# Kernel tuning notes

Hardware: AMD Instinct MI355X
Metric: run time of the kernel (lower is better)

Reference implementation:

```python
import jax, jax.numpy as jnp
import numpy as np
from jax import lax

B, C_IN, C_OUT, H, W, K, MID = 16, 256, 256, 64, 64, 3, 64
BN_EPS = 1e-5


def setup_inputs() -> dict:
    key = jax.random.key(0)
    ks = jax.random.split(key, 16)
    inp = {
        'x': jax.random.normal(ks[0], (B, C_IN, H, W), dtype=jnp.float32),
        # 4 kernel banks: (4, c2, c1//g, k, k)
        'weight': jax.random.normal(ks[1], (4, C_OUT, C_IN, K, K), dtype=jnp.float32) * 0.05,
        'gamma': jnp.ones((C_OUT,), jnp.float32),
        'beta': jnp.zeros((C_OUT,), jnp.float32),
    }
    # four attention branches: Linear(c, mid, bias=False) -> ReLU -> Linear(mid, 4, bias=True)
    names = ['s', 'c', 'f', 'w']
    for i, n in enumerate(names):
        inp[f'fc_{n}_w1'] = jax.random.normal(ks[2 + 3 * i], (MID, C_IN), dtype=jnp.float32) * 0.05
        inp[f'fc_{n}_w2'] = jax.random.normal(ks[3 + 3 * i], (4, MID), dtype=jnp.float32) * 0.05
        inp[f'fc_{n}_b2'] = jax.random.normal(ks[4 + 3 * i], (4,), dtype=jnp.float32) * 0.05
    return inp


def _branch(pooled, w1, w2, b2):
    # pooled: [B, C]; w1: [MID, C]; w2: [4, MID]
    h = jax.nn.relu(pooled @ w1.T)
    return jax.nn.softmax(h @ w2.T + b2, axis=1)  # [B, 4]


def reference(x, weight, gamma, beta,
              fc_s_w1, fc_s_w2, fc_s_b2,
              fc_c_w1, fc_c_w2, fc_c_b2,
              fc_f_w1, fc_f_w2, fc_f_b2,
              fc_w_w1, fc_w_w2, fc_w_b2):
    b = x.shape[0]
    pooled = jnp.mean(x, axis=(2, 3))  # GAP -> [B, C]
    alpha = (_branch(pooled, fc_s_w1, fc_s_w2, fc_s_b2)
             * _branch(pooled, fc_c_w1, fc_c_w2, fc_c_b2)
             * _branch(pooled, fc_f_w1, fc_f_w2, fc_f_b2)
             * _branch(pooled, fc_w_w1, fc_w_w2, fc_w_b2))  # [B, 4]
    # per-sample dynamic kernels: [B, out_c, in_c, k, k]
    dyn_w = jnp.einsum('bn,noikl->boikl', alpha, weight)

    def conv_one(xi, wi):
        # xi: [C, H, W]; wi: [out_c, in_c, k, k]
        return lax.conv_general_dilated(
            xi[None], wi, window_strides=(1, 1), padding='SAME',
            dimension_numbers=('NCHW', 'OIHW', 'NCHW'))[0]

    out = jax.vmap(conv_one)(x, dyn_w)  # [B, out_c, H, W]

    # BatchNorm2d (training-mode batch statistics)
    mean = jnp.mean(out, axis=(0, 2, 3))
    var = jnp.var(out, axis=(0, 2, 3))
    out = (out - mean[None, :, None, None]) * jax.lax.rsqrt(var + BN_EPS)[None, :, None, None]
    return out * gamma[None, :, None, None] + beta[None, :, None, None]
```

## Files before the change

### kernel.cpp

```cpp
#include <hip/hip_runtime.h>
#include <math.h>

#define BB 16
#define CIN 256
#define COUT 256
#define HH 64
#define WW 64
#define NBANK_STRIDE 589824

typedef short bf16x8 __attribute__((ext_vector_type(8)));
typedef float f32x4 __attribute__((ext_vector_type(4)));

#define WS_XT_OFF 32768
#define WS_DW_OFF 33587200
#define WS_NEED   52461568ULL

static __device__ __forceinline__ short f2bf(float f) {
    union { float f; unsigned u; } v; v.f = f;
    unsigned r = v.u + 0x7FFF + ((v.u >> 16) & 1);
    return (short)(r >> 16);
}

struct AttnParams {
    const float* w1[4];
    const float* w2[4];
    const float* b2[4];
};

__global__ __launch_bounds__(256) void xpose_kernel(const float* __restrict__ x,
                                                    short* __restrict__ xT,
                                                    float* __restrict__ pooled) {
    const int ci0 = blockIdx.x * 32;
    const int h0 = blockIdx.y * 4;
    const int b = blockIdx.z;
    const int t = threadIdx.x;
    __shared__ __align__(16) short tile[64][40];
    const int ci = t >> 3;
    const int l = t & 7;
    const int w = t >> 2;
    const int s4 = t & 3;
    float sacc = 0.f;
    for (int hh = 0; hh < 4; ++hh) {
        const int h = h0 + hh;
        __syncthreads();
        {
            const float4* src = (const float4*)(x + ((size_t)(b * 256 + ci0 + ci)) * 4096 + h * 64);
            float4 v1 = src[l * 2];
            float4 v2 = src[l * 2 + 1];
            tile[l * 8 + 0][ci] = f2bf(v1.x);
            tile[l * 8 + 1][ci] = f2bf(v1.y);
            tile[l * 8 + 2][ci] = f2bf(v1.z);
            tile[l * 8 + 3][ci] = f2bf(v1.w);
            tile[l * 8 + 4][ci] = f2bf(v2.x);
            tile[l * 8 + 5][ci] = f2bf(v2.y);
            tile[l * 8 + 6][ci] = f2bf(v2.z);
            tile[l * 8 + 7][ci] = f2bf(v2.w);
            sacc += v1.x + v1.y + v1.z + v1.w + v2.x + v2.y + v2.z + v2.w;
        }
        __syncthreads();
        {
            bf16x8 val = *(const bf16x8*)&tile[w][s4 * 8];
            *(bf16x8*)&xT[((size_t)b * 4096 + h * 64 + w) * 256 + ci0 + s4 * 8] = val;
        }
    }
    sacc += __shfl_xor(sacc, 1, 64);
    sacc += __shfl_xor(sacc, 2, 64);
    sacc += __shfl_xor(sacc, 4, 64);
    if (l == 0) atomicAdd(&pooled[b * 256 + ci0 + ci], sacc);
}

__global__ __launch_bounds__(256) void attn_kernel(AttnParams p, float* __restrict__ ws_f) {
    const int b = blockIdx.x;
    const int t = threadIdx.x;
    const int wv = t >> 6;
    const int lane = t & 63;
    __shared__ float ps[256];
    __shared__ float hs[4][64];
    __shared__ float lg[4][4];
    __shared__ float sm[4][4];
    ws_f[4096 + b * 256 + t] = 0.f;
    ps[t] = ws_f[b * 256 + t] * (1.0f / 4096.0f);
    __syncthreads();
    {
        const float4* w1v = (const float4*)(p.w1[wv] + lane * 256);
        float h = 0.f;
#pragma unroll 8
        for (int i = 0; i < 64; ++i) {
            float4 w4 = w1v[i];
            h += w4.x * ps[i * 4 + 0] + w4.y * ps[i * 4 + 1] +
                 w4.z * ps[i * 4 + 2] + w4.w * ps[i * 4 + 3];
        }
        hs[wv][lane] = fmaxf(h, 0.f);
    }
    __syncthreads();
    if (t < 16) {
        const int n = t >> 2, j = t & 3;
        const float* w2 = p.w2[n];
        float l = p.b2[n][j];
        for (int m = 0; m < 64; ++m) l += w2[j * 64 + m] * hs[n][m];
        lg[n][j] = l;
    }
    __syncthreads();
    if (t < 4) {
        const int n = t;
        float mx = fmaxf(fmaxf(lg[n][0], lg[n][1]), fmaxf(lg[n][2], lg[n][3]));
        float e0 = expf(lg[n][0] - mx), e1 = expf(lg[n][1] - mx);
        float e2 = expf(lg[n][2] - mx), e3 = expf(lg[n][3] - mx);
        float inv = 1.f / (e0 + e1 + e2 + e3);
        sm[n][0] = e0 * inv; sm[n][1] = e1 * inv; sm[n][2] = e2 * inv; sm[n][3] = e3 * inv;
    }
    __syncthreads();
    if (t < 4) ws_f[b * 256 + t] = sm[0][t] * sm[1][t] * sm[2][t] * sm[3][t];
}

__global__ __launch_bounds__(256) void dynw_kernel(const float* __restrict__ wt,
                                                   const float* __restrict__ ws_f,
                                                   short* __restrict__ dynwF) {
    const int co = blockIdx.x;
    const int ci = threadIdx.x;
    const int cotile = co >> 4;
    const int mh = co & 15;
    __shared__ __align__(16) short st[9][272];
    float w[4][9];
#pragma unroll
    for (int n = 0; n < 4; ++n) {
        const size_t base = ((size_t)(n * 256 + co) * 256 + ci) * 9;
#pragma unroll
        for (int k = 0; k < 9; ++k) w[n][k] = wt[base + k];
    }
    for (int b = 0; b < BB; ++b) {
        const float a0 = ws_f[b * 256 + 0];
        const float a1 = ws_f[b * 256 + 1];
        const float a2 = ws_f[b * 256 + 2];
        const float a3 = ws_f[b * 256 + 3];
#pragma unroll
        for (int k = 0; k < 9; ++k)
            st[k][ci] = f2bf(a0 * w[0][k] + a1 * w[1][k] + a2 * w[2][k] + a3 * w[3][k]);
        __syncthreads();
#pragma unroll
        for (int i = 0; i < 2; ++i) {
            const int task = ci + 256 * i;
            if (task < 288) {
                const int k = task >> 5;
                const int c5 = task & 31;
                const int cc = c5 >> 2;
                const int q = c5 & 3;
                bf16x8 v = *(const bf16x8*)&st[k][cc * 32 + q * 8];
                *(bf16x8*)&dynwF[((size_t)((b * 9 + k) * 16 + cotile) << 12) + cc * 512 + q * 128 + mh * 8] = v;
            }
        }
        __syncthreads();
    }
}

__global__ __launch_bounds__(256, 2) void conv_mfma_kernel(const short* __restrict__ xT,
                                                           const short* __restrict__ dynwF,
                                                           float* __restrict__ out,
                                                           float* __restrict__ bn_part) {
    const int id = blockIdx.x;
    const int xcd = id & 7;
    const int wi = id >> 3;
    const int b = xcd + ((wi >> 5) << 3);
    const int rem = wi & 31;
    const int mt = rem >> 4;
    const int nt = rem & 15;

    const int t = threadIdx.x;
    const int lane = t & 63;
    const int wv = t >> 6;
    const int wx = wv & 1;
    const int wy = wv >> 1;
    const int mh = lane & 15;
    const int q = lane >> 4;
    const int r0 = nt * 4;
    const int co0 = mt * 128;

    __shared__ __align__(16) short xs[396 * 64];
    __shared__ __align__(16) short As[2][4096];
    __shared__ float red[128][2][2];

    f32x4 acc[4][8];
#pragma unroll
    for (int i = 0; i < 4; ++i)
#pragma unroll
        for (int j = 0; j < 8; ++j) acc[i][j] = (f32x4){0.f, 0.f, 0.f, 0.f};

    const size_t a_b9 = (size_t)b * 9;
    const int a_ct = mt * 8 + (t >> 5);
    const int a_port16 = (t & 31) * 16;
    const int a_dst = (t >> 5) * 512 + a_port16;
    const int a_rd0 = (wy * 4) * 512 + lane * 8;

    const bf16x8 zero8 = {0, 0, 0, 0, 0, 0, 0, 0};

    for (int cc = 0; cc < 8; ++cc) {
        const int ci0 = cc * 32;
        __syncthreads();
        const short* asrc0 = dynwF + ((((a_b9 + 0) * 16 + a_ct) * 8 + cc) << 9) + a_port16;
        bf16x8 pa0 = *(const bf16x8*)(asrc0);
        bf16x8 pa1 = *(const bf16x8*)(asrc0 + 8);
#pragma unroll
        for (int i = 0; i < 7; ++i) {
            int idx = t + 256 * i;
            if (idx < 1584) {
                int p = idx >> 2;
                int sub = idx & 3;
                int lr = p / 66;
                int lc = p - lr * 66;
                int r = r0 - 1 + lr;
                int c = lc - 1;
                bf16x8 v = zero8;
                if ((unsigned)r < 64u && (unsigned)c < 64u)
                    v = *(const bf16x8*)&xT[((size_t)b * 4096 + r * 64 + c) * 256 + ci0 + sub * 8];
                *(bf16x8*)&xs[(p << 6) + ((sub ^ (p & 7)) << 3)] = v;
            }
        }
        *(bf16x8*)&As[0][a_dst] = pa0;
        *(bf16x8*)&As[0][a_dst + 8] = pa1;
        __syncthreads();
#pragma unroll
        for (int khw = 0; khw < 9; ++khw) {
            const int kh = khw / 3;
            const int kw = khw - kh * 3;
            bf16x8 na0, na1;
            if (khw < 8) {
                const short* s = dynwF + ((((a_b9 + khw + 1) * 16 + a_ct) * 8 + cc) << 9) + a_port16;
                na0 = *(const bf16x8*)(s);
                na1 = *(const bf16x8*)(s + 8);
            }
            bf16x8 bfr[8];
#pragma unroll
            for (int ni = 0; ni < 8; ++ni) {
                const int row_l = wx * 2 + (ni >> 2) + kh;
                const int col_l = (ni & 3) * 16 + kw + mh;
                const int pp = row_l * 66 + col_l;
                bfr[ni] = *(const bf16x8*)&xs[(pp << 6) + ((q ^ (pp & 7)) << 3)];
            }
#pragma unroll
            for (int mi = 0; mi < 4; ++mi) {
                bf16x8 af = *(const bf16x8*)&As[khw & 1][a_rd0 + mi * 512];
#pragma unroll
                for (int ni = 0; ni < 8; ++ni)
                    acc[mi][ni] = __builtin_amdgcn_mfma_f32_16x16x32_bf16(af, bfr[ni], acc[mi][ni], 0, 0, 0);
            }
            if (khw < 8) {
                *(bf16x8*)&As[(khw + 1) & 1][a_dst] = na0;
                *(bf16x8*)&As[(khw + 1) & 1][a_dst + 8] = na1;
                __syncthreads();
            }
        }
    }

    float s16[4][4], q16[4][4];
#pragma unroll
    for (int mi = 0; mi < 4; ++mi)
#pragma unroll
        for (int reg = 0; reg < 4; ++reg) { s16[mi][reg] = 0.f; q16[mi][reg] = 0.f; }

#pragma unroll
    for (int mi = 0; mi < 4; ++mi) {
#pragma unroll
        for (int ni = 0; ni < 8; ++ni) {
            const int pix = wx * 128 + ni * 16 + mh;
            const int h = r0 + (pix >> 6);
            const int w = pix & 63;
#pragma unroll
            for (int reg = 0; reg < 4; ++reg) {
                const int co = co0 + wy * 64 + mi * 16 + q * 4 + reg;
                const float e = acc[mi][ni][reg];
                out[(((size_t)b * 256 + co) << 12) + (h << 6) + w] = e;
                s16[mi][reg] += e;
                q16[mi][reg] += e * e;
            }
        }
    }
#pragma unroll
    for (int mi = 0; mi < 4; ++mi)
#pragma unroll
        for (int reg = 0; reg < 4; ++reg) {
            float s = s16[mi][reg], sq = q16[mi][reg];
            s += __shfl_xor(s, 1, 64);  sq += __shfl_xor(sq, 1, 64);
            s += __shfl_xor(s, 2, 64);  sq += __shfl_xor(sq, 2, 64);
            s += __shfl_xor(s, 4, 64);  sq += __shfl_xor(sq, 4, 64);
            s += __shfl_xor(s, 8, 64);  sq += __shfl_xor(sq, 8, 64);
            if (mh == 0) {
                const int co_l = wy * 64 + mi * 16 + q * 4 + reg;
                red[co_l][0][wx] = s;
                red[co_l][1][wx] = sq;
            }
        }
    __syncthreads();
    {
        const int co_l = t >> 1;
        const int st = t & 1;
        float v = red[co_l][st][0] + red[co_l][st][1];
        atomicAdd(&bn_part[(st * 256 + co0 + co_l) * 8 + (nt & 7)], v);
    }
}

__global__ __launch_bounds__(256) void bn_apply_kernel(float* __restrict__ out,
                                                       const float* __restrict__ bn_part,
                                                       const float* __restrict__ gamma,
                                                       const float* __restrict__ beta) {
    const int gid = blockIdx.x * 256 + threadIdx.x;
    const int c = (blockIdx.x >> 2) & 255;
    float S = 0.f, Q = 0.f;
#pragma unroll
    for (int s = 0; s < 8; ++s) {
        S += bn_part[c * 8 + s];
        Q += bn_part[(256 + c) * 8 + s];
    }
    const float mean = S * (1.f / 65536.f);
    const float var = Q * (1.f / 65536.f) - mean * mean;
    const float inv = rsqrtf(var + 1e-5f);
    const float sc = gamma[c] * inv;
    const float sh = beta[c] - mean * sc;
    float4* p = (float4*)out;
    float4 v = p[gid];
    v.x = v.x * sc + sh;
    v.y = v.y * sc + sh;
    v.z = v.z * sc + sh;
    v.w = v.w * sc + sh;
    p[gid] = v;
}

__global__ __launch_bounds__(256) void gap_kernel(const float* __restrict__ x,
                                                  float* __restrict__ pooled) {
    const int plane = blockIdx.x;
    const float4* p = (const float4*)(x + (size_t)plane * 4096);
    const int t = threadIdx.x;
    float s = 0.f;
#pragma unroll
    for (int i = 0; i < 4; ++i) {
        float4 v = p[t + 256 * i];
        s += v.x + v.y + v.z + v.w;
    }
#pragma unroll
    for (int off = 32; off > 0; off >>= 1) s += __shfl_down(s, off, 64);
    __shared__ float red[4];
    if ((t & 63) == 0) red[t >> 6] = s;
    __syncthreads();
    if (t == 0) pooled[plane] = (red[0] + red[1] + red[2] + red[3]) * (1.0f / 4096.0f);
}

__global__ __launch_bounds__(64) void attn64_kernel(const float* __restrict__ pooled,
                                                    AttnParams p,
                                                    float* __restrict__ alpha) {
    const int b = blockIdx.x;
    const int t = threadIdx.x;
    __shared__ float ps[256];
    __shared__ float hs[64];
    __shared__ float lg[4];
    __shared__ float prod[4];
#pragma unroll
    for (int i = 0; i < 4; ++i) ps[t + 64 * i] = pooled[b * 256 + t + 64 * i];
    if (t < 4) prod[t] = 1.f;
    __syncthreads();
    for (int n = 0; n < 4; ++n) {
        const float* w1 = p.w1[n];
        float h = 0.f;
        for (int c = 0; c < 256; ++c) h += w1[t * 256 + c] * ps[c];
        hs[t] = fmaxf(h, 0.f);
        __syncthreads();
        if (t < 4) {
            const float* w2 = p.w2[n];
            float l = p.b2[n][t];
            for (int m = 0; m < 64; ++m) l += w2[t * 64 + m] * hs[m];
            lg[t] = l;
        }
        __syncthreads();
        if (t == 0) {
            float mx = fmaxf(fmaxf(lg[0], lg[1]), fmaxf(lg[2], lg[3]));
            float e0 = expf(lg[0] - mx), e1 = expf(lg[1] - mx);
            float e2 = expf(lg[2] - mx), e3 = expf(lg[3] - mx);
            float inv = 1.f / (e0 + e1 + e2 + e3);
            prod[0] *= e0 * inv; prod[1] *= e1 * inv;
            prod[2] *= e2 * inv; prod[3] *= e3 * inv;
        }
        __syncthreads();
    }
    if (t < 4) alpha[b * 4 + t] = prod[t];
}

__global__ __launch_bounds__(256) void conv_fp32_kernel(const float* __restrict__ x,
                                                        const float* __restrict__ wt,
                                                        const float* __restrict__ alpha,
                                                        float* __restrict__ out) {
    const int h = blockIdx.x;
    const int cot = blockIdx.y;
    const int b = blockIdx.z;
    const int t = threadIdx.x;
    const int tx = t & 15;
    const int ty = t >> 4;
    const int co0 = cot * 64;
    __shared__ __align__(16) float xsf[32][68];
    __shared__ __align__(16) float wshf[3][32][68];
    const float a0 = alpha[b * 4 + 0], a1 = alpha[b * 4 + 1];
    const float a2 = alpha[b * 4 + 2], a3 = alpha[b * 4 + 3];
    float acc[4][4];
#pragma unroll
    for (int i = 0; i < 4; ++i)
#pragma unroll
        for (int j = 0; j < 4; ++j) acc[i][j] = 0.f;
    const size_t xbase = (size_t)b * CIN * 4096;
    for (int kh = 0; kh < 3; ++kh) {
        const int r = h + kh - 1;
        if (r < 0 || r >= HH) continue;
        for (int chunk = 0; chunk < 8; ++chunk) {
            const int ci0 = chunk * 32;
            __syncthreads();
#pragma unroll
            for (int i = 0; i < 8; ++i) {
                int flat = t + 256 * i;
                int ci = flat >> 6;
                int w = flat & 63;
                xsf[ci][1 + w] = x[xbase + (size_t)(ci0 + ci) * 4096 + r * 64 + w];
            }
            if (t < 32) { xsf[t][0] = 0.f; xsf[t][65] = 0.f; xsf[t][66] = 0.f; xsf[t][67] = 0.f; }
#pragma unroll
            for (int j = 0; j < 24; ++j) {
                int e = t + 256 * j;
                int co = e / 96;
                int rem = e - co * 96;
                int ci = rem / 3;
                int kw = rem - ci * 3;
                size_t g = (((size_t)(co0 + co) * 256 + (ci0 + ci)) * 3 + kh) * 3 + kw;
                wshf[kw][ci][co] = a0 * wt[g] + a1 * wt[g + NBANK_STRIDE] +
                                   a2 * wt[g + 2 * NBANK_STRIDE] + a3 * wt[g + 3 * NBANK_STRIDE];
            }
            __syncthreads();
            for (int ci = 0; ci < 32; ++ci) {
                float4 w0 = *(const float4*)&wshf[0][ci][tx * 4];
                float4 w1v = *(const float4*)&wshf[1][ci][tx * 4];
                float4 w2v = *(const float4*)&wshf[2][ci][tx * 4];
                float4 xa = *(const float4*)&xsf[ci][ty * 4];
                float4 xb = *(const float4*)&xsf[ci][ty * 4 + 4];
                float v[8] = {xa.x, xa.y, xa.z, xa.w, xb.x, xb.y, xb.z, xb.w};
                float aw[3][4] = {{w0.x, w0.y, w0.z, w0.w},
                                  {w1v.x, w1v.y, w1v.z, w1v.w},
                                  {w2v.x, w2v.y, w2v.z, w2v.w}};
#pragma unroll
                for (int kw = 0; kw < 3; ++kw)
#pragma unroll
                    for (int i = 0; i < 4; ++i)
#pragma unroll
                        for (int j = 0; j < 4; ++j)
                            acc[i][j] += aw[kw][i] * v[j + kw];
            }
        }
    }
    size_t obase = (((size_t)b * COUT + co0 + tx * 4) * 64 + h) * 64 + ty * 4;
#pragma unroll
    for (int i = 0; i < 4; ++i) {
        float4 o = {acc[i][0], acc[i][1], acc[i][2], acc[i][3]};
        *(float4*)&out[obase + (size_t)i * 4096] = o;
    }
}

__global__ __launch_bounds__(256) void bn_stats_kernel(const float* __restrict__ out,
                                                       const float* __restrict__ gamma,
                                                       const float* __restrict__ beta,
                                                       float* __restrict__ scale,
                                                       float* __restrict__ shift) {
    const int co = blockIdx.x;
    const int t = threadIdx.x;
    float s = 0.f, sq = 0.f;
    for (int b = 0; b < BB; ++b) {
        const float4* p = (const float4*)(out + ((size_t)b * 256 + co) * 4096);
#pragma unroll
        for (int i = 0; i < 4; ++i) {
            float4 v = p[t + 256 * i];
            s += v.x + v.y + v.z + v.w;
            sq += v.x * v.x + v.y * v.y + v.z * v.z + v.w * v.w;
        }
    }
#pragma unroll
    for (int off = 32; off > 0; off >>= 1) {
        s += __shfl_down(s, off, 64);
        sq += __shfl_down(sq, off, 64);
    }
    __shared__ float rs[4], rq[4];
    if ((t & 63) == 0) { rs[t >> 6] = s; rq[t >> 6] = sq; }
    __syncthreads();
    if (t == 0) {
        float S = rs[0] + rs[1] + rs[2] + rs[3];
        float Q = rq[0] + rq[1] + rq[2] + rq[3];
        float mean = S * (1.f / 65536.f);
        float var = Q * (1.f / 65536.f) - mean * mean;
        float inv = rsqrtf(var + 1e-5f);
        float sc = gamma[co] * inv;
        scale[co] = sc;
        shift[co] = beta[co] - mean * sc;
    }
}

__global__ __launch_bounds__(256) void bn_apply_sc_kernel(float* __restrict__ out,
                                                          const float* __restrict__ scale,
                                                          const float* __restrict__ shift) {
    const int gid = blockIdx.x * 256 + threadIdx.x;
    const int c = (gid >> 10) & 255;
    float4* p = (float4*)out;
    float4 v = p[gid];
    const float sc = scale[c], sh = shift[c];
    v.x = v.x * sc + sh;
    v.y = v.y * sc + sh;
    v.z = v.z * sc + sh;
    v.w = v.w * sc + sh;
    p[gid] = v;
}

extern "C" void kernel_launch(void* const* d_in, const int* in_sizes, int n_in,
                              void* d_out, int out_size, void* d_ws, size_t ws_size,
                              hipStream_t stream) {
    (void)in_sizes; (void)n_in; (void)out_size;
    const float* x = (const float*)d_in[0];
    const float* wt = (const float*)d_in[1];
    const float* gamma = (const float*)d_in[2];
    const float* beta = (const float*)d_in[3];
    AttnParams ap;
    for (int n = 0; n < 4; ++n) {
        ap.w1[n] = (const float*)d_in[4 + 3 * n];
        ap.w2[n] = (const float*)d_in[5 + 3 * n];
        ap.b2[n] = (const float*)d_in[6 + 3 * n];
    }
    float* ws_f = (float*)d_ws;
    float* out = (float*)d_out;

    if (ws_size >= WS_NEED) {
        short* xT = (short*)((char*)d_ws + WS_XT_OFF);
        short* dynwF = (short*)((char*)d_ws + WS_DW_OFF);
        float* bn_part = ws_f + 4096;

        hipMemsetAsync(d_ws, 0, 32768, stream);
        xpose_kernel<<<dim3(8, 16, 16), 256, 0, stream>>>(x, xT, ws_f);
        attn_kernel<<<16, 256, 0, stream>>>(ap, ws_f);
        dynw_kernel<<<256, 256, 0, stream>>>(wt, ws_f, dynwF);
        conv_mfma_kernel<<<512, 256, 0, stream>>>(xT, dynwF, out, bn_part);
        bn_apply_kernel<<<16384, 256, 0, stream>>>(out, bn_part, gamma, beta);
    } else {
        float* pooled = ws_f;
        float* alpha = ws_f + 4096;
        float* scale = ws_f + 4160;
        float* shift = ws_f + 4416;
        gap_kernel<<<4096, 256, 0, stream>>>(x, pooled);
        attn64_kernel<<<16, 64, 0, stream>>>(pooled, ap, alpha);
        conv_fp32_kernel<<<dim3(64, 4, 16), 256, 0, stream>>>(x, wt, alpha, out);
        bn_stats_kernel<<<256, 256, 0, stream>>>(out, gamma, beta, scale, shift);
        bn_apply_sc_kernel<<<16384, 256, 0, stream>>>(out, scale, shift);
    }
}
```

Measured before the change: 272.3 us.

## Fuse BatchNorm apply into conv kernel via grid-wide atomic barrier

The conv kernel now holds its accumulators in registers, publishes per-channel sum and sum-of-squares partials, then waits on a global atomic counter until all 512 blocks have contributed. Each block then computes the scale and shift for its channels and writes the normalized output directly. This removes the separate bn_apply pass, which read and wrote the whole 64 MB output a second time. The grid barrier assumes all 512 blocks are co-resident (2 per CU on 256 CUs), which risks deadlock if occupancy is lower. The counter lives in a workspace slot that is zeroed by the memset and also cleared in attn_kernel.

Result: slower. 291.0 us (+6.9%).

```diff
diff --git a/kernel.cpp b/kernel.cpp
--- a/kernel.cpp
+++ b/kernel.cpp
@@ -81,6 +81,7 @@
     ws_f[4096 + b * 256 + t] = 0.f;
     ps[t] = ws_f[b * 256 + t] * (1.0f / 4096.0f);
     __syncthreads();
+    if (b == 0 && t == 8) ws_f[8] = 0.f;
     {
         const float4* w1v = (const float4*)(p.w1[wv] + lane * 256);
         float h = 0.f;
@@ -156,7 +157,10 @@
 __global__ __launch_bounds__(256, 2) void conv_mfma_kernel(const short* __restrict__ xT,
                                                            const short* __restrict__ dynwF,
                                                            float* __restrict__ out,
-                                                           float* __restrict__ bn_part) {
+                                                           float* __restrict__ bn_part,
+                                                           const float* __restrict__ gamma,
+                                                           const float* __restrict__ beta,
+                                                           int* __restrict__ cnt) {
     const int id = blockIdx.x;
     const int xcd = id & 7;
     const int wi = id >> 3;
@@ -258,22 +262,15 @@
         for (int reg = 0; reg < 4; ++reg) { s16[mi][reg] = 0.f; q16[mi][reg] = 0.f; }
 
 #pragma unroll
-    for (int mi = 0; mi < 4; ++mi) {
-#pragma unroll
-        for (int ni = 0; ni < 8; ++ni) {
-            const int pix = wx * 128 + ni * 16 + mh;
-            const int h = r0 + (pix >> 6);
-            const int w = pix & 63;
+    for (int mi = 0; mi < 4; ++mi)
+#pragma unroll
+        for (int ni = 0; ni < 8; ++ni)
 #pragma unroll
             for (int reg = 0; reg < 4; ++reg) {
-                const int co = co0 + wy * 64 + mi * 16 + q * 4 + reg;
                 const float e = acc[mi][ni][reg];
-                out[(((size_t)b * 256 + co) << 12) + (h << 6) + w] = e;
                 s16[mi][reg] += e;
                 q16[mi][reg] += e * e;
             }
-        }
-    }
 #pragma unroll
     for (int mi = 0; mi < 4; ++mi)
 #pragma unroll
@@ -296,32 +293,49 @@
         float v = red[co_l][st][0] + red[co_l][st][1];
         atomicAdd(&bn_part[(st * 256 + co0 + co_l) * 8 + (nt & 7)], v);
     }
-}
-
-__global__ __launch_bounds__(256) void bn_apply_kernel(float* __restrict__ out,
-                                                       const float* __restrict__ bn_part,
-                                                       const float* __restrict__ gamma,
-                                                       const float* __restrict__ beta) {
-    const int gid = blockIdx.x * 256 + threadIdx.x;
-    const int c = (blockIdx.x >> 2) & 255;
-    float S = 0.f, Q = 0.f;
-#pragma unroll
-    for (int s = 0; s < 8; ++s) {
-        S += bn_part[c * 8 + s];
-        Q += bn_part[(256 + c) * 8 + s];
-    }
-    const float mean = S * (1.f / 65536.f);
-    const float var = Q * (1.f / 65536.f) - mean * mean;
-    const float inv = rsqrtf(var + 1e-5f);
-    const float sc = gamma[c] * inv;
-    const float sh = beta[c] - mean * sc;
-    float4* p = (float4*)out;
-    float4 v = p[gid];
-    v.x = v.x * sc + sh;
-    v.y = v.y * sc + sh;
-    v.z = v.z * sc + sh;
-    v.w = v.w * sc + sh;
-    p[gid] = v;
+    __syncthreads();
+
+    if (t == 0) {
+        __threadfence();
+        atomicAdd(cnt, 1);
+        while (__hip_atomic_load(cnt, __ATOMIC_ACQUIRE, __HIP_MEMORY_SCOPE_AGENT) < 512)
+            __builtin_amdgcn_s_sleep(8);
+    }
+    __syncthreads();
+
+    float* scsh = &red[0][0][0];
+    if (t < 128) {
+        const int co = co0 + t;
+        float S = 0.f, Q = 0.f;
+#pragma unroll
+        for (int s = 0; s < 8; ++s) {
+            S += __hip_atomic_load(&bn_part[co * 8 + s], __ATOMIC_RELAXED, __HIP_MEMORY_SCOPE_AGENT);
+            Q += __hip_atomic_load(&bn_part[(256 + co) * 8 + s], __ATOMIC_RELAXED, __HIP_MEMORY_SCOPE_AGENT);
+        }
+        const float mean = S * (1.f / 65536.f);
+        const float var = Q * (1.f / 65536.f) - mean * mean;
+        const float inv = rsqrtf(var + 1e-5f);
+        const float sc = gamma[co] * inv;
+        scsh[t * 2] = sc;
+        scsh[t * 2 + 1] = beta[co] - mean * sc;
+    }
+    __syncthreads();
+
+#pragma unroll
+    for (int mi = 0; mi < 4; ++mi) {
+#pragma unroll
+        for (int ni = 0; ni < 8; ++ni) {
+            const int pix = wx * 128 + ni * 16 + mh;
+            const int h = r0 + (pix >> 6);
+            const int w = pix & 63;
+#pragma unroll
+            for (int reg = 0; reg < 4; ++reg) {
+                const int co_l = wy * 64 + mi * 16 + q * 4 + reg;
+                const float e = acc[mi][ni][reg] * scsh[co_l * 2] + scsh[co_l * 2 + 1];
+                out[(((size_t)b * 256 + co0 + co_l) << 12) + (h << 6) + w] = e;
+            }
+        }
+    }
 }
 
 __global__ __launch_bounds__(256) void gap_kernel(const float* __restrict__ x,
@@ -530,13 +544,13 @@
         short* xT = (short*)((char*)d_ws + WS_XT_OFF);
         short* dynwF = (short*)((char*)d_ws + WS_DW_OFF);
         float* bn_part = ws_f + 4096;
+        int* cnt = (int*)(ws_f + 8);
 
         hipMemsetAsync(d_ws, 0, 32768, stream);
         xpose_kernel<<<dim3(8, 16, 16), 256, 0, stream>>>(x, xT, ws_f);
         attn_kernel<<<16, 256, 0, stream>>>(ap, ws_f);
         dynw_kernel<<<256, 256, 0, stream>>>(wt, ws_f, dynwF);
-        conv_mfma_kernel<<<512, 256, 0, stream>>>(xT, dynwF, out, bn_part);
-        bn_apply_kernel<<<16384, 256, 0, stream>>>(out, bn_part, gamma, beta);
+        conv_mfma_kernel<<<512, 256, 0, stream>>>(xT, dynwF, out, bn_part, gamma, beta, cnt);
     } else {
         float* pooled = ws_f;
         float* alpha = ws_f + 4096;
```

## Load dynamic-weight fragments directly to registers, drop LDS A staging

Applied to the files above, without the earlier changes.

The weight (A) operand was previously staged through a double-buffered LDS tile with a barrier after every kernel tap. It is now loaded straight from global memory into registers, using two register sets in ping-pong with a two-tap prefetch distance. This removes eight barriers per channel chunk and the LDS write/read traffic for A. In exchange it uses more VGPRs and relies on the weight layout being arranged so each lane's fragment is contiguous, with the global load latency now hidden only by the MFMA work of the preceding taps.

New measurement: 393.7 us. 1.45x slower.

```diff
diff --git a/kernel.cpp b/kernel.cpp
--- a/kernel.cpp
+++ b/kernel.cpp
@@ -176,7 +176,6 @@
     const int co0 = mt * 128;
 
     __shared__ __align__(16) short xs[396 * 64];
-    __shared__ __align__(16) short As[2][4096];
     __shared__ float red[128][2][2];
 
     f32x4 acc[4][8];
@@ -186,70 +185,87 @@
         for (int j = 0; j < 8; ++j) acc[i][j] = (f32x4){0.f, 0.f, 0.f, 0.f};
 
     const size_t a_b9 = (size_t)b * 9;
-    const int a_ct = mt * 8 + (t >> 5);
-    const int a_port16 = (t & 31) * 16;
-    const int a_dst = (t >> 5) * 512 + a_port16;
-    const int a_rd0 = (wy * 4) * 512 + lane * 8;
+    const int a_cot0 = mt * 8 + wy * 4;
+    const short* Aw = dynwF + lane * 8;
+
+#define LOAD_A(dst, k, c)                                                             \
+    {                                                                                 \
+        _Pragma("unroll")                                                             \
+        for (int mi = 0; mi < 4; ++mi)                                                \
+            dst[mi] = *(const bf16x8*)(Aw + ((((a_b9 + (k)) * 16 + a_cot0 + mi) * 8 + (c)) << 9)); \
+    }
+
+    bf16x8 afA[4], afB[4];
+    LOAD_A(afA, 0, 0);
+    LOAD_A(afB, 1, 0);
 
     const bf16x8 zero8 = {0, 0, 0, 0, 0, 0, 0, 0};
 
-    for (int cc = 0; cc < 8; ++cc) {
-        const int ci0 = cc * 32;
-        __syncthreads();
-        const short* asrc0 = dynwF + ((((a_b9 + 0) * 16 + a_ct) * 8 + cc) << 9) + a_port16;
-        bf16x8 pa0 = *(const bf16x8*)(asrc0);
-        bf16x8 pa1 = *(const bf16x8*)(asrc0 + 8);
-#pragma unroll
-        for (int i = 0; i < 7; ++i) {
-            int idx = t + 256 * i;
-            if (idx < 1584) {
-                int p = idx >> 2;
-                int sub = idx & 3;
-                int lr = p / 66;
-                int lc = p - lr * 66;
-                int r = r0 - 1 + lr;
-                int c = lc - 1;
-                bf16x8 v = zero8;
-                if ((unsigned)r < 64u && (unsigned)c < 64u)
-                    v = *(const bf16x8*)&xT[((size_t)b * 4096 + r * 64 + c) * 256 + ci0 + sub * 8];
-                *(bf16x8*)&xs[(p << 6) + ((sub ^ (p & 7)) << 3)] = v;
-            }
-        }
-        *(bf16x8*)&As[0][a_dst] = pa0;
-        *(bf16x8*)&As[0][a_dst + 8] = pa1;
-        __syncthreads();
-#pragma unroll
-        for (int khw = 0; khw < 9; ++khw) {
-            const int kh = khw / 3;
-            const int kw = khw - kh * 3;
-            bf16x8 na0, na1;
-            if (khw < 8) {
-                const short* s = dynwF + ((((a_b9 + khw + 1) * 16 + a_ct) * 8 + cc) << 9) + a_port16;
-                na0 = *(const bf16x8*)(s);
-                na1 = *(const bf16x8*)(s + 8);
-            }
-            bf16x8 bfr[8];
-#pragma unroll
-            for (int ni = 0; ni < 8; ++ni) {
-                const int row_l = wx * 2 + (ni >> 2) + kh;
-                const int col_l = (ni & 3) * 16 + kw + mh;
-                const int pp = row_l * 66 + col_l;
-                bfr[ni] = *(const bf16x8*)&xs[(pp << 6) + ((q ^ (pp & 7)) << 3)];
-            }
-#pragma unroll
-            for (int mi = 0; mi < 4; ++mi) {
-                bf16x8 af = *(const bf16x8*)&As[khw & 1][a_rd0 + mi * 512];
-#pragma unroll
-                for (int ni = 0; ni < 8; ++ni)
-                    acc[mi][ni] = __builtin_amdgcn_mfma_f32_16x16x32_bf16(af, bfr[ni], acc[mi][ni], 0, 0, 0);
-            }
-            if (khw < 8) {
-                *(bf16x8*)&As[(khw + 1) & 1][a_dst] = na0;
-                *(bf16x8*)&As[(khw + 1) & 1][a_dst + 8] = na1;
-                __syncthreads();
-            }
-        }
-    }
+    for (int ccp = 0; ccp < 4; ++ccp) {
+#pragma unroll
+        for (int half = 0; half < 2; ++half) {
+            const int cc = ccp * 2 + half;
+            const int ci0 = cc * 32;
+            __syncthreads();
+#pragma unroll
+            for (int i = 0; i < 7; ++i) {
+                int idx = t + 256 * i;
+                if (idx < 1584) {
+                    int p = idx >> 2;
+                    int sub = idx & 3;
+                    int lr = p / 66;
+                    int lc = p - lr * 66;
+                    int r = r0 - 1 + lr;
+                    int c = lc - 1;
+                    bf16x8 v = zero8;
+                    if ((unsigned)r < 64u && (unsigned)c < 64u)
+                        v = *(const bf16x8*)&xT[((size_t)b * 4096 + r * 64 + c) * 256 + ci0 + sub * 8];
+                    *(bf16x8*)&xs[(p << 6) + ((sub ^ (p & 7)) << 3)] = v;
+                }
+            }
+            __syncthreads();
+#pragma unroll
+            for (int khw = 0; khw < 9; ++khw) {
+                const int kh = khw / 3;
+                const int kw = khw - kh * 3;
+                const int par = (half + khw) & 1;
+
+                bf16x8 bfr[8];
+#pragma unroll
+                for (int ni = 0; ni < 8; ++ni) {
+                    const int row_l = wx * 2 + (ni >> 2) + kh;
+                    const int col_l = (ni & 3) * 16 + kw + mh;
+                    const int pp = row_l * 66 + col_l;
+                    bfr[ni] = *(const bf16x8*)&xs[(pp << 6) + ((q ^ (pp & 7)) << 3)];
+                }
+
+                if (par == 0) {
+#pragma unroll
+                    for (int mi = 0; mi < 4; ++mi)
+#pragma unroll
+                        for (int ni = 0; ni < 8; ++ni)
+                            acc[mi][ni] = __builtin_amdgcn_mfma_f32_16x16x32_bf16(afA[mi], bfr[ni], acc[mi][ni], 0, 0, 0);
+                    if (!(cc == 7 && khw >= 7)) {
+                        const int nk = (khw < 7) ? (khw + 2) : (khw - 7);
+                        const int ncc = (khw < 7) ? cc : (cc + 1);
+                        LOAD_A(afA, nk, ncc);
+                    }
+                } else {
+#pragma unroll
+                    for (int mi = 0; mi < 4; ++mi)
+#pragma unroll
+                        for (int ni = 0; ni < 8; ++ni)
+                            acc[mi][ni] = __builtin_amdgcn_mfma_f32_16x16x32_bf16(afB[mi], bfr[ni], acc[mi][ni], 0, 0, 0);
+                    if (!(cc == 7 && khw >= 7)) {
+                        const int nk = (khw < 7) ? (khw + 2) : (khw - 7);
+                        const int ncc = (khw < 7) ? cc : (cc + 1);
+                        LOAD_A(afB, nk, ncc);
+                    }
+                }
+            }
+        }
+    }
+#undef LOAD_A
 
     float s16[4][4], q16[4][4];
 #pragma unroll
```
